# Performance work log

Measured on AMD Instinct MI355X. Metric: run time of the kernel, lower is better.

The kernel has to match this reference:

```python
import jax, jax.numpy as jnp
import numpy as np

SEQ_LEN = 8192
HIDDEN = 2048


def setup_inputs() -> dict:
    key = jax.random.key(0)
    ks = jax.random.split(key, 7)
    scale = 1.0 / np.sqrt(HIDDEN)
    return {
        "hidden": jax.random.normal(ks[0], (1, HIDDEN), dtype=jnp.float32),
        "encoder_outputs": jax.random.normal(ks[1], (SEQ_LEN, HIDDEN), dtype=jnp.float32),
        "pool_output": jax.random.normal(ks[2], (1, HIDDEN), dtype=jnp.float32),
        # nn.Linear(hidden, hidden) params for attn_pool_q and attn_q_hidden
        "W_pq": jax.random.uniform(ks[3], (HIDDEN, HIDDEN), jnp.float32, -scale, scale),
        "b_pq": jax.random.uniform(ks[4], (HIDDEN,), jnp.float32, -scale, scale),
        "W_qh": jax.random.uniform(ks[5], (HIDDEN, HIDDEN), jnp.float32, -scale, scale),
        "b_qh": jax.random.uniform(ks[6], (HIDDEN,), jnp.float32, -scale, scale),
    }


def reference(hidden, encoder_outputs, pool_output, W_pq, b_pq, W_qh, b_qh):
    # Batched form of the original per-step 'general' score loop:
    #   e_i = hidden . ( W_qh @ (enc_i * (W_pq @ pool + b_pq)) + b_qh )
    m = pool_output.reshape(-1) @ W_pq.T + b_pq          # (H,)  attn_pool_q(pool)
    gated = encoder_outputs * m[None, :]                 # (S, H) enc_i * energy
    e = gated @ W_qh.T + b_qh                            # (S, H) attn_q_hidden(.)
    energies = e @ hidden.reshape(-1)                    # (S,)  dot with hidden
    # F.softmax over the seq dim, then .unsqueeze(0).unsqueeze(0) -> (1,1,S)
    return jax.nn.softmax(energies)[None, None, :]
```

## Files before the change

kernel.cpp:

```cpp
#include <hip/hip_runtime.h>
#include <math.h>

#define SEQ 8192
#define HID 2048
#define NC4 (HID / 4)
#define VCHUNKS 8


__global__ __launch_bounds__(256) void k1(const float* __restrict__ pool,
                                          const float* __restrict__ W_pq,
                                          const float* __restrict__ b_pq,
                                          const float* __restrict__ hidden,
                                          const float* __restrict__ W_qh,
                                          float* __restrict__ m,
                                          float* __restrict__ vpart) {
  const int tid  = threadIdx.x;
  const int wave = tid >> 6;
  const int lane = tid & 63;
  const int bid  = blockIdx.x;

  if (bid < 256) {
    const float4* p4 = reinterpret_cast<const float4*>(pool);
    #pragma unroll
    for (int rr = 0; rr < 2; ++rr) {
      const int row = bid * 8 + wave * 2 + rr;
      const float4* Wrow = reinterpret_cast<const float4*>(W_pq + (size_t)row * HID);
      float acc = 0.f;
      #pragma unroll
      for (int i = lane; i < NC4; i += 64) {
        float4 w = Wrow[i], p = p4[i];
        acc += w.x * p.x + w.y * p.y + w.z * p.z + w.w * p.w;
      }
      #pragma unroll
      for (int off = 32; off; off >>= 1) acc += __shfl_down(acc, off, 64);
      if (lane == 0) m[row] = acc + b_pq[row];
    }
  } else {
    __shared__ float4 part[256];
    const int u  = bid - 256;
    const int ct = u & 31;
    const int rc = u >> 5;
    const int c4 = ct * 16 + (tid & 15);
    const int r0 = rc * 256 + (tid >> 4) * 16;
    float4 acc = {0.f, 0.f, 0.f, 0.f};
    #pragma unroll
    for (int i = 0; i < 16; ++i) {
      const int r = r0 + i;
      const float h  = hidden[r];
      const float4 w = reinterpret_cast<const float4*>(W_qh + (size_t)r * HID)[c4];
      acc.x += h * w.x; acc.y += h * w.y; acc.z += h * w.z; acc.w += h * w.w;
    }
    part[tid] = acc;
    __syncthreads();
    if (tid < 16) {
      float4 s = part[tid];
      #pragma unroll
      for (int k = 1; k < 16; ++k) {
        float4 p = part[k * 16 + tid];
        s.x += p.x; s.y += p.y; s.z += p.z; s.w += p.w;
      }
      reinterpret_cast<float4*>(vpart)[rc * NC4 + ct * 16 + tid] = s;
    }
  }
}

__global__ __launch_bounds__(256) void k2(const float* __restrict__ enc,
                                          const float* __restrict__ m,
                                          const float* __restrict__ vpart,
                                          float* __restrict__ energ) {
  __shared__ float4 gl[NC4];
  const int tid  = threadIdx.x;
  const int wave = tid >> 6;
  const int lane = tid & 63;
  const int bid  = blockIdx.x;

  const float4* vp = reinterpret_cast<const float4*>(vpart);
  const float4* m4 = reinterpret_cast<const float4*>(m);
  #pragma unroll
  for (int j = 0; j < 2; ++j) {
    const int c = tid + j * 256;
    float4 a = vp[c];
    #pragma unroll
    for (int k = 1; k < VCHUNKS; ++k) {
      float4 p = vp[k * NC4 + c];
      a.x += p.x; a.y += p.y; a.z += p.z; a.w += p.w;
    }
    const float4 mm = m4[c];
    float4 g = {a.x * mm.x, a.y * mm.y, a.z * mm.z, a.w * mm.w};
    gl[c] = g;
  }
  __syncthreads();

  #pragma unroll
  for (int rr = 0; rr < 4; ++rr) {
    const int row = bid * 16 + wave * 4 + rr;
    const float4* E = reinterpret_cast<const float4*>(enc + (size_t)row * HID);
    float acc = 0.f;
    #pragma unroll
    for (int i = lane; i < NC4; i += 64) {
      float4 e = E[i], g = gl[i];
      acc += e.x * g.x + e.y * g.y + e.z * g.z + e.w * g.w;
    }
    #pragma unroll
    for (int off = 32; off; off >>= 1) acc += __shfl_down(acc, off, 64);
    if (lane == 0) energ[row] = acc;
  }
}

__global__ __launch_bounds__(256) void k3(const float* __restrict__ e,
                                          float* __restrict__ out) {
  __shared__ float red[8];
  const int tid  = threadIdx.x;
  const int wave = tid >> 6;
  const int lane = tid & 63;
  const int bid  = blockIdx.x;

  float vals[32];
  float mx = -INFINITY;
  #pragma unroll
  for (int i = 0; i < 32; ++i) {
    vals[i] = e[tid + i * 256];
    mx = fmaxf(mx, vals[i]);
  }
  #pragma unroll
  for (int off = 32; off; off >>= 1) mx = fmaxf(mx, __shfl_down(mx, off, 64));
  if (lane == 0) red[wave] = mx;
  __syncthreads();
  const float bm = fmaxf(fmaxf(red[0], red[1]), fmaxf(red[2], red[3]));

  float s = 0.f;
  #pragma unroll
  for (int i = 0; i < 32; ++i) s += expf(vals[i] - bm);
  #pragma unroll
  for (int off = 32; off; off >>= 1) s += __shfl_down(s, off, 64);
  if (lane == 0) red[4 + wave] = s;
  __syncthreads();
  const float inv = 1.f / (red[4] + red[5] + red[6] + red[7]);

  const int row = bid * 256 + tid;
  out[row] = expf(e[row] - bm) * inv;
}

extern "C" void kernel_launch(void* const* d_in, const int* in_sizes, int n_in,
                              void* d_out, int out_size, void* d_ws, size_t ws_size,
                              hipStream_t stream) {
  const float* hidden = (const float*)d_in[0];
  const float* enc    = (const float*)d_in[1];
  const float* pool   = (const float*)d_in[2];
  const float* W_pq   = (const float*)d_in[3];
  const float* b_pq   = (const float*)d_in[4];
  const float* W_qh   = (const float*)d_in[5];

  float* out   = (float*)d_out;
  float* ws    = (float*)d_ws;
  float* m     = ws;
  float* vpart = ws + HID;
  float* energ = ws + HID + VCHUNKS * HID;

  k1<<<dim3(512), dim3(256), 0, stream>>>(pool, W_pq, b_pq, hidden, W_qh, m, vpart);
  k2<<<dim3(512), dim3(256), 0, stream>>>(enc, m, vpart, energ);
  k3<<<dim3(32), dim3(256), 0, stream>>>(energ, out);
}
```

Baseline: 27.13 us.

## Fuse softmax into energy kernel via last-block atomic counter

Removes the separate softmax launch: each k2 block bumps a global atomic counter after writing its energies, and the last block to finish runs the full softmax over all 8192 energies. The counter is reset in k1. It also keeps the gated vector in registers and processes two encoder rows at a time to add memory-level parallelism. In exchange, the softmax runs on a single block (32 blocks before), serialised at the tail, and the change adds fences and an atomic per block.

New measurement: 79.16 us. +191.8%, slower.

```diff
diff --git a/kernel.cpp b/kernel.cpp
--- a/kernel.cpp
+++ b/kernel.cpp
@@ -5,6 +5,7 @@
 #define HID 2048
 #define NC4 (HID / 4)
 #define VCHUNKS 8
+#define NBK2 512
 
 
 __global__ __launch_bounds__(256) void k1(const float* __restrict__ pool,
@@ -13,11 +14,14 @@
                                           const float* __restrict__ hidden,
                                           const float* __restrict__ W_qh,
                                           float* __restrict__ m,
-                                          float* __restrict__ vpart) {
+                                          float* __restrict__ vpart,
+                                          unsigned* __restrict__ counter) {
   const int tid  = threadIdx.x;
   const int wave = tid >> 6;
   const int lane = tid & 63;
   const int bid  = blockIdx.x;
+
+  if (bid == 0 && tid == 0) *counter = 0u;
 
   if (bid < 256) {
     const float4* p4 = reinterpret_cast<const float4*>(pool);
@@ -67,8 +71,12 @@
 __global__ __launch_bounds__(256) void k2(const float* __restrict__ enc,
                                           const float* __restrict__ m,
                                           const float* __restrict__ vpart,
-                                          float* __restrict__ energ) {
+                                          float* __restrict__ energ,
+                                          unsigned* __restrict__ counter,
+                                          float* __restrict__ out) {
   __shared__ float4 gl[NC4];
+  __shared__ float red[8];
+  __shared__ unsigned oldv;
   const int tid  = threadIdx.x;
   const int wave = tid >> 6;
   const int lane = tid & 63;
@@ -91,35 +99,45 @@
   }
   __syncthreads();
 
+  float4 greg[8];
   #pragma unroll
-  for (int rr = 0; rr < 4; ++rr) {
-    const int row = bid * 16 + wave * 4 + rr;
-    const float4* E = reinterpret_cast<const float4*>(enc + (size_t)row * HID);
-    float acc = 0.f;
+  for (int j = 0; j < 8; ++j) greg[j] = gl[lane + j * 64];
+
+  #pragma unroll
+  for (int rp = 0; rp < 2; ++rp) {
+    const int row0 = bid * 16 + wave * 4 + rp * 2;
+    const float4* E0 = reinterpret_cast<const float4*>(enc + (size_t)row0 * HID);
+    const float4* E1 = reinterpret_cast<const float4*>(enc + (size_t)(row0 + 1) * HID);
+    float acc0 = 0.f, acc1 = 0.f;
     #pragma unroll
-    for (int i = lane; i < NC4; i += 64) {
-      float4 e = E[i], g = gl[i];
-      acc += e.x * g.x + e.y * g.y + e.z * g.z + e.w * g.w;
+    for (int j = 0; j < 8; ++j) {
+      const int i = lane + j * 64;
+      float4 e0 = E0[i], e1 = E1[i], g = greg[j];
+      acc0 += e0.x * g.x + e0.y * g.y + e0.z * g.z + e0.w * g.w;
+      acc1 += e1.x * g.x + e1.y * g.y + e1.z * g.z + e1.w * g.w;
     }
     #pragma unroll
-    for (int off = 32; off; off >>= 1) acc += __shfl_down(acc, off, 64);
-    if (lane == 0) energ[row] = acc;
+    for (int off = 32; off; off >>= 1) {
+      acc0 += __shfl_down(acc0, off, 64);
+      acc1 += __shfl_down(acc1, off, 64);
+    }
+    if (lane == 0) {
+      energ[row0]     = acc0;
+      energ[row0 + 1] = acc1;
+    }
   }
-}
 
-__global__ __launch_bounds__(256) void k3(const float* __restrict__ e,
-                                          float* __restrict__ out) {
-  __shared__ float red[8];
-  const int tid  = threadIdx.x;
-  const int wave = tid >> 6;
-  const int lane = tid & 63;
-  const int bid  = blockIdx.x;
+  __threadfence();
+  if (tid == 0) oldv = atomicAdd(counter, 1u);
+  __syncthreads();
+  if (oldv != NBK2 - 1) return;
 
+  __threadfence();
   float vals[32];
   float mx = -INFINITY;
   #pragma unroll
   for (int i = 0; i < 32; ++i) {
-    vals[i] = e[tid + i * 256];
+    vals[i] = energ[tid + i * 256];
     mx = fmaxf(mx, vals[i]);
   }
   #pragma unroll
@@ -130,15 +148,18 @@
 
   float s = 0.f;
   #pragma unroll
-  for (int i = 0; i < 32; ++i) s += expf(vals[i] - bm);
+  for (int i = 0; i < 32; ++i) {
+    vals[i] = expf(vals[i] - bm);
+    s += vals[i];
+  }
   #pragma unroll
   for (int off = 32; off; off >>= 1) s += __shfl_down(s, off, 64);
   if (lane == 0) red[4 + wave] = s;
   __syncthreads();
   const float inv = 1.f / (red[4] + red[5] + red[6] + red[7]);
 
-  const int row = bid * 256 + tid;
-  out[row] = expf(e[row] - bm) * inv;
+  #pragma unroll
+  for (int i = 0; i < 32; ++i) out[tid + i * 256] = vals[i] * inv;
 }
 
 extern "C" void kernel_launch(void* const* d_in, const int* in_sizes, int n_in,
@@ -151,13 +172,14 @@
   const float* b_pq   = (const float*)d_in[4];
   const float* W_qh   = (const float*)d_in[5];
 
-  float* out   = (float*)d_out;
-  float* ws    = (float*)d_ws;
-  float* m     = ws;
-  float* vpart = ws + HID;
-  float* energ = ws + HID + VCHUNKS * HID;
+  float*    out     = (float*)d_out;
+  float*    ws      = (float*)d_ws;
+  float*    m       = ws;
+  float*    vpart   = ws + HID;
+  float*    energ   = ws + HID + VCHUNKS * HID;
+  unsigned* counter = (unsigned*)(ws + HID + VCHUNKS * HID + SEQ);
 
-  k1<<<dim3(512), dim3(256), 0, stream>>>(pool, W_pq, b_pq, hidden, W_qh, m, vpart);
-  k2<<<dim3(512), dim3(256), 0, stream>>>(enc, m, vpart, energ);
-  k3<<<dim3(32), dim3(256), 0, stream>>>(energ, out);
+  k1<<<dim3(512), dim3(256), 0, stream>>>(pool, W_pq, b_pq, hidden, W_qh,
+                                          m, vpart, counter);
+  k2<<<dim3(NBK2), dim3(256), 0, stream>>>(enc, m, vpart, energ, counter, out);
 }
```
